# Kernel tuning notes

Measured on AMD Instinct MI355X. Metric: run time of the kernel, lower is better.

## Reference

```python
import jax, jax.numpy as jnp
import numpy as np

N = 50000       # nodes
E = 800000      # edges
IN, H, OUT = 256, 512, 64


def gcn_conv(x, src, dst, norm, W, b, n_nodes):
    # PyG GCNConv: linear transform first, then normalized scatter-add aggregation.
    xw = x @ W                                   # [N, H]
    msg = xw[src] * norm[:, None]                # [E+N, H] gathered, normalized messages
    out = jax.ops.segment_sum(msg, dst, num_segments=n_nodes)
    return out + b


def setup_inputs() -> dict:
    key = jax.random.key(0)
    ks = jax.random.split(key, 8)
    x = jax.random.normal(ks[0], (N, IN), dtype=jnp.float32)
    edge_index = jax.random.randint(ks[1], (2, E), 0, N, dtype=jnp.int64)
    W1 = jax.random.normal(ks[2], (IN, H), dtype=jnp.float32) * (1.0 / np.sqrt(IN))
    b1 = jnp.zeros((H,), dtype=jnp.float32)
    W2 = jax.random.normal(ks[3], (H, H), dtype=jnp.float32) * (1.0 / np.sqrt(H))
    b2 = jnp.zeros((H,), dtype=jnp.float32)
    Wl = jax.random.normal(ks[4], (H, OUT), dtype=jnp.float32) * (1.0 / np.sqrt(H))
    bl = jnp.zeros((OUT,), dtype=jnp.float32)
    return {"x": x, "edge_index": edge_index, "W1": W1, "b1": b1,
            "W2": W2, "b2": b2, "Wl": Wl, "bl": bl}


def reference(x, edge_index, W1, b1, W2, b2, Wl, bl):
    n = x.shape[0]
    loop = jnp.arange(n, dtype=edge_index.dtype)
    src = jnp.concatenate([edge_index[0], loop])     # add self-loops
    dst = jnp.concatenate([edge_index[1], loop])
    # symmetric normalization D^-1/2 (A+I) D^-1/2
    deg = jax.ops.segment_sum(jnp.ones_like(dst, dtype=x.dtype), dst, num_segments=n)
    dinv = jnp.where(deg > 0, jax.lax.rsqrt(jnp.maximum(deg, 1.0)), 0.0)
    norm = dinv[src] * dinv[dst]                      # [E+N]

    h = jax.nn.relu(gcn_conv(x, src, dst, norm, W1, b1, n))
    # dropout omitted (deterministic eval reference)
    h = jax.nn.relu(gcn_conv(h, src, dst, norm, W2, b2, n))
    return h @ Wl + bl
```

## Files before the change

kernel.cpp:

```cpp
#include <hip/hip_runtime.h>
#include <cstdint>
#include <cstddef>

typedef unsigned short u16;
typedef __attribute__((ext_vector_type(8))) _Float16 f16x8;
typedef __attribute__((ext_vector_type(4))) float f32x4;
typedef __attribute__((ext_vector_type(2))) unsigned u32x2;
typedef __attribute__((ext_vector_type(4))) unsigned u32x4;

__device__ __forceinline__ u16 f2h(float f) {
    union { _Float16 h; u16 u; } v; v.h = (_Float16)f;
    return v.u;
}
__device__ __forceinline__ float h2f(u16 b) {
    union { u16 u; _Float16 h; } v; v.u = b;
    return (float)v.h;
}
__device__ __forceinline__ float h2f_lo(unsigned w) { return h2f((u16)(w & 0xFFFFu)); }
__device__ __forceinline__ float h2f_hi(unsigned w) { return h2f((u16)(w >> 16)); }

__device__ __forceinline__ void gload16(const u16* g, u16* l) {
    __builtin_amdgcn_global_load_lds(
        (const __attribute__((address_space(1))) void*)g,
        (__attribute__((address_space(3))) void*)l, 16, 0, 0);
}

__global__ void init_deg_kernel(float* __restrict__ deg, int n) {
    int i = blockIdx.x * blockDim.x + threadIdx.x;
    if (i < n) deg[i] = 1.0f;
}

__global__ void count_deg_kernel(const int* __restrict__ dst, float* __restrict__ deg, int e) {
    int i = blockIdx.x * blockDim.x + threadIdx.x;
    if (i < e) atomicAdd(&deg[dst[i]], 1.0f);
}

__global__ __launch_bounds__(1024)
void scan1_kernel(const float* __restrict__ deg, int* __restrict__ part, int n) {
    __shared__ int sm[1024];
    const int t = threadIdx.x;
    const int i = blockIdx.x * 1024 + t;
    sm[t] = (i < n) ? (int)deg[i] - 1 : 0;
    __syncthreads();
    for (int off = 512; off > 0; off >>= 1) {
        if (t < off) sm[t] += sm[t + off];
        __syncthreads();
    }
    if (t == 0) part[blockIdx.x] = sm[0];
}

__global__ __launch_bounds__(1024)
void scan2_kernel(int* __restrict__ part, int nb) {
    __shared__ int sm[1024];
    const int t = threadIdx.x;
    const int v = (t < nb) ? part[t] : 0;
    sm[t] = v;
    __syncthreads();
    for (int off = 1; off < 1024; off <<= 1) {
        int tv = (t >= off) ? sm[t - off] : 0;
        __syncthreads();
        sm[t] += tv;
        __syncthreads();
    }
    if (t < nb) part[t] = sm[t] - v;
}

__global__ __launch_bounds__(1024)
void scan3_kernel(const float* __restrict__ deg, const int* __restrict__ part,
                  float* __restrict__ dinv, int* __restrict__ row_start,
                  int* __restrict__ cursor, int n) {
    __shared__ int sm[1024];
    const int t = threadIdx.x;
    const int b = blockIdx.x;
    const int i = b * 1024 + t;
    int v = 0;
    float d = 1.f;
    if (i < n) {
        d = deg[i];
        v = (int)d - 1;
    }
    sm[t] = v;
    __syncthreads();
    for (int off = 1; off < 1024; off <<= 1) {
        int tv = (t >= off) ? sm[t - off] : 0;
        __syncthreads();
        sm[t] += tv;
        __syncthreads();
    }
    if (i < n) {
        row_start[i] = part[b] + sm[t] - v;
        dinv[i] = rsqrtf(d);
        cursor[i] = 0;
    }
    if (i == n - 1) row_start[n] = part[b] + sm[t];
}

__global__ void bucket_kernel(const int* __restrict__ src, const int* __restrict__ dst,
                              const int* __restrict__ row_start, int* __restrict__ cursor,
                              int* __restrict__ csr, float* __restrict__ csr_w,
                              const float* __restrict__ dinv, int e) {
    int i = blockIdx.x * blockDim.x + threadIdx.x;
    if (i < e) {
        int d = dst[i];
        int s = src[i];
        int pos = atomicAdd(&cursor[d], 1);
        int at = row_start[d] + pos;
        csr[at] = s;
        csr_w[at] = dinv[s] * dinv[d];
    }
}

__global__ void wtrans_kernel(const float* __restrict__ W, u16* __restrict__ bt, int K, int N) {
    const int k8 = K >> 3;
    const int idx = blockIdx.x * blockDim.x + threadIdx.x;
    if (idx >= N * k8) return;
    const int n = idx / k8;
    const int k0 = (idx - n * k8) * 8;
    alignas(16) u16 h8[8];
#pragma unroll
    for (int j = 0; j < 8; j++) h8[j] = f2h(W[(size_t)(k0 + j) * N + n]);
    *(uint4*)(bt + (size_t)n * K + k0) = *(const uint4*)h8;
}

__global__ void xsplit_kernel(const float* __restrict__ x, u16* __restrict__ xh, size_t total8) {
    const size_t idx = (size_t)blockIdx.x * blockDim.x + threadIdx.x;
    if (idx >= total8) return;
    const float4 v0 = *(const float4*)(x + idx * 8);
    const float4 v1 = *(const float4*)(x + idx * 8 + 4);
    alignas(16) u16 h8[8];
    h8[0] = f2h(v0.x); h8[1] = f2h(v0.y); h8[2] = f2h(v0.z); h8[3] = f2h(v0.w);
    h8[4] = f2h(v1.x); h8[5] = f2h(v1.y); h8[6] = f2h(v1.z); h8[7] = f2h(v1.w);
    *(uint4*)(xh + idx * 8) = *(const uint4*)h8;
}

__global__ __launch_bounds__(256)
void agg_x_kernel(const float* __restrict__ x, const u16* __restrict__ xh,
                  u16* __restrict__ oh,
                  const int* __restrict__ csr, const float* __restrict__ csr_w,
                  const int* __restrict__ rs, const float* __restrict__ dinv, int n) {
    const int node = blockIdx.x * 4 + (threadIdx.x >> 6);
    if (node >= n) return;
    const int lane = threadIdx.x & 63;
    const int c0 = lane * 4;
    const int beg = rs[node], end = rs[node + 1];
    float a0 = 0.f, a1 = 0.f, a2 = 0.f, a3 = 0.f;
    int i = beg;
    for (; i + 4 <= end; i += 4) {
        int s[4];
        float w[4];
        uint2 hv[4];
#pragma unroll
        for (int u = 0; u < 4; u++) {
            s[u] = __builtin_nontemporal_load(csr + i + u);
            w[u] = __builtin_nontemporal_load(csr_w + i + u);
        }
#pragma unroll
        for (int u = 0; u < 4; u++) hv[u] = *(const uint2*)(xh + (size_t)s[u] * 256 + c0);
#pragma unroll
        for (int u = 0; u < 4; u++) {
            a0 = fmaf(h2f_lo(hv[u].x), w[u], a0);
            a1 = fmaf(h2f_hi(hv[u].x), w[u], a1);
            a2 = fmaf(h2f_lo(hv[u].y), w[u], a2);
            a3 = fmaf(h2f_hi(hv[u].y), w[u], a3);
        }
    }
    for (; i < end; i++) {
        const int sv = csr[i];
        const float w = csr_w[i];
        uint2 hv = *(const uint2*)(xh + (size_t)sv * 256 + c0);
        a0 = fmaf(h2f_lo(hv.x), w, a0);
        a1 = fmaf(h2f_hi(hv.x), w, a1);
        a2 = fmaf(h2f_lo(hv.y), w, a2);
        a3 = fmaf(h2f_hi(hv.y), w, a3);
    }
    {
        const float dn = dinv[node];
        const float ws = dn * dn;
        const float4 xv = *(const float4*)(x + (size_t)node * 256 + c0);
        a0 = fmaf(xv.x, ws, a0);
        a1 = fmaf(xv.y, ws, a1);
        a2 = fmaf(xv.z, ws, a2);
        a3 = fmaf(xv.w, ws, a3);
    }
    u32x2 ho;
    ho.x = (unsigned)f2h(a0) | ((unsigned)f2h(a1) << 16);
    ho.y = (unsigned)f2h(a2) | ((unsigned)f2h(a3) << 16);
    __builtin_nontemporal_store(ho, (u32x2*)(oh + (size_t)node * 256 + c0));
}

__global__ __launch_bounds__(256)
void agg_h_kernel(const u16* __restrict__ hin, u16* __restrict__ oh,
                  const int* __restrict__ csr, const float* __restrict__ csr_w,
                  const int* __restrict__ rs, const float* __restrict__ dinv, int n) {
    const int node = blockIdx.x * 4 + (threadIdx.x >> 6);
    if (node >= n) return;
    const int lane = threadIdx.x & 63;
    const int c0 = lane * 8;
    const int beg = rs[node], end = rs[node + 1];
    float a[8];
#pragma unroll
    for (int j = 0; j < 8; j++) a[j] = 0.f;
    int i = beg;
    for (; i + 4 <= end; i += 4) {
        int s[4];
        float w[4];
        uint4 hv[4];
#pragma unroll
        for (int u = 0; u < 4; u++) {
            s[u] = __builtin_nontemporal_load(csr + i + u);
            w[u] = __builtin_nontemporal_load(csr_w + i + u);
        }
#pragma unroll
        for (int u = 0; u < 4; u++) hv[u] = *(const uint4*)(hin + (size_t)s[u] * 512 + c0);
#pragma unroll
        for (int u = 0; u < 4; u++) {
            a[0] = fmaf(h2f_lo(hv[u].x), w[u], a[0]);
            a[1] = fmaf(h2f_hi(hv[u].x), w[u], a[1]);
            a[2] = fmaf(h2f_lo(hv[u].y), w[u], a[2]);
            a[3] = fmaf(h2f_hi(hv[u].y), w[u], a[3]);
            a[4] = fmaf(h2f_lo(hv[u].z), w[u], a[4]);
            a[5] = fmaf(h2f_hi(hv[u].z), w[u], a[5]);
            a[6] = fmaf(h2f_lo(hv[u].w), w[u], a[6]);
            a[7] = fmaf(h2f_hi(hv[u].w), w[u], a[7]);
        }
    }
    for (; i < end; i++) {
        const int sv = csr[i];
        const float w = csr_w[i];
        uint4 hv = *(const uint4*)(hin + (size_t)sv * 512 + c0);
        a[0] = fmaf(h2f_lo(hv.x), w, a[0]);
        a[1] = fmaf(h2f_hi(hv.x), w, a[1]);
        a[2] = fmaf(h2f_lo(hv.y), w, a[2]);
        a[3] = fmaf(h2f_hi(hv.y), w, a[3]);
        a[4] = fmaf(h2f_lo(hv.z), w, a[4]);
        a[5] = fmaf(h2f_hi(hv.z), w, a[5]);
        a[6] = fmaf(h2f_lo(hv.w), w, a[6]);
        a[7] = fmaf(h2f_hi(hv.w), w, a[7]);
    }
    {
        const float dn = dinv[node];
        const float ws = dn * dn;
        uint4 hv = *(const uint4*)(hin + (size_t)node * 512 + c0);
        a[0] = fmaf(h2f_lo(hv.x), ws, a[0]);
        a[1] = fmaf(h2f_hi(hv.x), ws, a[1]);
        a[2] = fmaf(h2f_lo(hv.y), ws, a[2]);
        a[3] = fmaf(h2f_hi(hv.y), ws, a[3]);
        a[4] = fmaf(h2f_lo(hv.z), ws, a[4]);
        a[5] = fmaf(h2f_hi(hv.z), ws, a[5]);
        a[6] = fmaf(h2f_lo(hv.w), ws, a[6]);
        a[7] = fmaf(h2f_hi(hv.w), ws, a[7]);
    }
    u32x4 ho;
#pragma unroll
    for (int j = 0; j < 4; j++)
        ho[j] = (unsigned)f2h(a[2 * j]) | ((unsigned)f2h(a[2 * j + 1]) << 16);
    __builtin_nontemporal_store(ho, (u32x4*)(oh + (size_t)node * 512 + c0));
}

template <bool RELU, int OUTMODE>
__global__ __launch_bounds__(512)
void gemm256_kernel(const u16* __restrict__ A, const u16* __restrict__ Bt,
                    const float* __restrict__ bias,
                    float* __restrict__ Cf, u16* __restrict__ Ch,
                    int M, int K, int Nn) {
    __shared__ u16 sA[128 * 32], sB[256 * 32];

    const int gx = gridDim.x;
    const int nwg = gx * gridDim.y;
    const int orig = blockIdx.y * gx + blockIdx.x;
    const int q8 = nwg >> 3, r8 = nwg & 7;
    const int xcd = orig & 7, lin = orig >> 3;
    const int wg = (xcd < r8 ? xcd * (q8 + 1) : r8 * (q8 + 1) + (xcd - r8) * q8) + lin;
    const int mt = wg / gx;
    const int nt = wg - mt * gx;
    const int m0 = mt * 128, n0 = nt * 256;

    const int tid = threadIdx.x;
    const int lane = tid & 63;
    const int wid = tid >> 6;
    const int wm = (wid >> 2) * 64;
    const int wn = (wid & 3) * 64;

    const int srow = tid >> 2;
    const int gslot = (tid & 3) ^ ((tid >> 3) & 3);
    const int lbase = wid * 16 * 32;

    const u16* gA  = A  + (size_t)(m0 + srow) * K + gslot * 8;
    const u16* gB0 = Bt + (size_t)(n0 + srow) * K + gslot * 8;
    const u16* gB1 = Bt + (size_t)(n0 + 128 + srow) * K + gslot * 8;

    int offA[4], offB[4];
    const int q = lane >> 4;
#pragma unroll
    for (int i = 0; i < 4; i++) {
        int r = wm + i * 16 + (lane & 15);
        offA[i] = r * 32 + ((q ^ ((r >> 1) & 3)) * 8);
    }
#pragma unroll
    for (int j = 0; j < 4; j++) {
        int r = wn + j * 16 + (lane & 15);
        offB[j] = r * 32 + ((q ^ ((r >> 1) & 3)) * 8);
    }

    f32x4 acc[4][4];
#pragma unroll
    for (int i = 0; i < 4; i++)
#pragma unroll
        for (int j = 0; j < 4; j++) acc[i][j] = (f32x4){0.f, 0.f, 0.f, 0.f};

    auto stage = [&](int k0) {
        gload16(gA + k0, sA + lbase);
        gload16(gB0 + k0, sB + lbase);
        gload16(gB1 + k0, sB + 128 * 32 + lbase);
    };

    stage(0);
    for (int k0 = 0; k0 < K; k0 += 32) {
        __syncthreads();
        f16x8 af[4], bf[4];
#pragma unroll
        for (int i = 0; i < 4; i++) af[i] = *(const f16x8*)(sA + offA[i]);
#pragma unroll
        for (int j = 0; j < 4; j++) bf[j] = *(const f16x8*)(sB + offB[j]);
#pragma unroll
        for (int i = 0; i < 4; i++)
#pragma unroll
            for (int j = 0; j < 4; j++)
                acc[i][j] = __builtin_amdgcn_mfma_f32_16x16x32_f16(af[i], bf[j], acc[i][j], 0, 0, 0);
        __syncthreads();
        if (k0 + 32 < K) stage(k0 + 32);
    }

    const int cn = lane & 15;
    const int cm = (lane >> 4) * 4;
#pragma unroll
    for (int i = 0; i < 4; i++) {
#pragma unroll
        for (int j = 0; j < 4; j++) {
            const int col = n0 + wn + j * 16 + cn;
            const float bv = bias[col];
#pragma unroll
            for (int r = 0; r < 4; r++) {
                const int row = m0 + wm + i * 16 + cm + r;
                if (row < M) {
                    float v = acc[i][j][r] + bv;
                    if (RELU) v = fmaxf(v, 0.f);
                    if constexpr (OUTMODE == 2) {
                        Ch[(size_t)row * Nn + col] = f2h(v);
                    } else {
                        Cf[(size_t)row * Nn + col] = v;
                    }
                }
            }
        }
    }
}

template <bool RELU>
__global__ __launch_bounds__(256)
void gemm64_kernel(const u16* __restrict__ A, const u16* __restrict__ Bt,
                   const float* __restrict__ bias, float* __restrict__ Cf,
                   int M, int K, int Nn) {
    __shared__ u16 sA[128 * 32], sB[64 * 32];

    const int nwg = gridDim.y;
    const int orig = blockIdx.y;
    const int q8 = nwg >> 3, r8 = nwg & 7;
    const int xcd = orig & 7, lin = orig >> 3;
    const int wg = (xcd < r8 ? xcd * (q8 + 1) : r8 * (q8 + 1) + (xcd - r8) * q8) + lin;
    const int m0 = wg * 128, n0 = 0;

    const int tid = threadIdx.x;
    const int lane = tid & 63;
    const int wid = tid >> 6;
    const int wm = (wid >> 1) * 64;
    const int wn = (wid & 1) * 32;

    const int srow = tid >> 2;
    const int gslot = (tid & 3) ^ ((tid >> 3) & 3);
    const int lbase = wid * 16 * 32;

    const u16* gA0 = A + (size_t)(m0 + srow) * K + gslot * 8;
    const u16* gA1 = A + (size_t)(m0 + 64 + srow) * K + gslot * 8;
    const u16* gB0 = Bt + (size_t)(n0 + srow) * K + gslot * 8;

    int offA[4], offB[2];
    const int q = lane >> 4;
#pragma unroll
    for (int i = 0; i < 4; i++) {
        int r = wm + i * 16 + (lane & 15);
        offA[i] = r * 32 + ((q ^ ((r >> 1) & 3)) * 8);
    }
#pragma unroll
    for (int j = 0; j < 2; j++) {
        int r = wn + j * 16 + (lane & 15);
        offB[j] = r * 32 + ((q ^ ((r >> 1) & 3)) * 8);
    }

    f32x4 acc[4][2];
#pragma unroll
    for (int i = 0; i < 4; i++)
#pragma unroll
        for (int j = 0; j < 2; j++) acc[i][j] = (f32x4){0.f, 0.f, 0.f, 0.f};

    auto stage = [&](int k0) {
        gload16(gA0 + k0, sA + lbase);
        gload16(gA1 + k0, sA + 64 * 32 + lbase);
        gload16(gB0 + k0, sB + lbase);
    };

    stage(0);
    for (int k0 = 0; k0 < K; k0 += 32) {
        __syncthreads();
        f16x8 af[4], bf[2];
#pragma unroll
        for (int i = 0; i < 4; i++) af[i] = *(const f16x8*)(sA + offA[i]);
#pragma unroll
        for (int j = 0; j < 2; j++) bf[j] = *(const f16x8*)(sB + offB[j]);
#pragma unroll
        for (int i = 0; i < 4; i++)
#pragma unroll
            for (int j = 0; j < 2; j++)
                acc[i][j] = __builtin_amdgcn_mfma_f32_16x16x32_f16(af[i], bf[j], acc[i][j], 0, 0, 0);
        __syncthreads();
        if (k0 + 32 < K) stage(k0 + 32);
    }

    const int cn = lane & 15;
    const int cm = (lane >> 4) * 4;
#pragma unroll
    for (int i = 0; i < 4; i++) {
#pragma unroll
        for (int j = 0; j < 2; j++) {
            const int col = wn + j * 16 + cn;
            const float bv = bias[col];
#pragma unroll
            for (int r = 0; r < 4; r++) {
                const int row = m0 + wm + i * 16 + cm + r;
                if (row < M) {
                    float v = acc[i][j][r] + bv;
                    if (RELU) v = fmaxf(v, 0.f);
                    Cf[(size_t)row * Nn + col] = v;
                }
            }
        }
    }
}

extern "C" void kernel_launch(void* const* d_in, const int* in_sizes, int n_in,
                              void* d_out, int out_size, void* d_ws, size_t ws_size,
                              hipStream_t stream) {
    const float* x  = (const float*)d_in[0];
    const int*   ei = (const int*)d_in[1];
    const float* W1 = (const float*)d_in[2];
    const float* b1 = (const float*)d_in[3];
    const float* W2 = (const float*)d_in[4];
    const float* b2 = (const float*)d_in[5];
    const float* Wl = (const float*)d_in[6];
    const float* bl = (const float*)d_in[7];
    float* out = (float*)d_out;

    const int N = in_sizes[0] / 256;
    const int E = in_sizes[1] / 2;
    const int Mpad = ((N + 127) / 128) * 128;
    const int nb = (N + 1023) / 1024;
    const int* src = ei;
    const int* dst = ei + E;

    size_t off = 0;
    auto alloc = [&](size_t bytes) -> void* {
        void* p = (char*)d_ws + off;
        off += (bytes + 255) & ~(size_t)255;
        return p;
    };
    float* deg       = (float*)alloc((size_t)N * 4);
    float* dinv      = (float*)alloc((size_t)N * 4);
    int*   part      = (int*)alloc((size_t)1024 * 4);
    int*   row_start = (int*)alloc((size_t)(N + 1) * 4);
    int*   cursor    = (int*)alloc((size_t)N * 4);
    int*   csr       = (int*)alloc((size_t)E * 4);
    float* csr_w     = (float*)alloc((size_t)E * 4);
    u16*   xh        = (u16*)alloc((size_t)N * 256 * 2);
    u16*   bt1 = (u16*)alloc((size_t)512 * 256 * 2);
    u16*   bt2 = (u16*)alloc((size_t)512 * 512 * 2);
    u16*   bt3 = (u16*)alloc((size_t)64 * 512 * 2);
    u16*   slabA = (u16*)alloc((size_t)Mpad * 512 * 2);
    u16*   slabH = (u16*)alloc((size_t)Mpad * 512 * 2);
    (void)ws_size;

    u16* a1h = slabA;
    u16* a2h = slabA;
    u16* h1h = slabH;
    u16* h2h = slabH;

    init_deg_kernel<<<(N + 255) / 256, 256, 0, stream>>>(deg, N);
    count_deg_kernel<<<(E + 255) / 256, 256, 0, stream>>>(dst, deg, E);
    scan1_kernel<<<nb, 1024, 0, stream>>>(deg, part, N);
    scan2_kernel<<<1, 1024, 0, stream>>>(part, nb);
    scan3_kernel<<<nb, 1024, 0, stream>>>(deg, part, dinv, row_start, cursor, N);
    bucket_kernel<<<(E + 255) / 256, 256, 0, stream>>>(src, dst, row_start, cursor, csr, csr_w, dinv, E);

    wtrans_kernel<<<(512 * 32 + 255) / 256, 256, 0, stream>>>(W1, bt1, 256, 512);
    wtrans_kernel<<<(512 * 64 + 255) / 256, 256, 0, stream>>>(W2, bt2, 512, 512);
    wtrans_kernel<<<(64 * 64 + 255) / 256, 256, 0, stream>>>(Wl, bt3, 512, 64);
    xsplit_kernel<<<((N * 32) + 255) / 256, 256, 0, stream>>>(x, xh, (size_t)N * 32);

    agg_x_kernel<<<(N + 3) / 4, 256, 0, stream>>>(x, xh, a1h, csr, csr_w, row_start, dinv, N);
    gemm256_kernel<true, 2><<<dim3(2, Mpad / 128), 512, 0, stream>>>(
        a1h, bt1, b1, nullptr, h1h, N, 256, 512);

    agg_h_kernel<<<(N + 3) / 4, 256, 0, stream>>>(h1h, a2h, csr, csr_w, row_start, dinv, N);
    gemm256_kernel<true, 2><<<dim3(2, Mpad / 128), 512, 0, stream>>>(
        a2h, bt2, b2, nullptr, h2h, N, 512, 512);

    gemm64_kernel<false><<<dim3(1, Mpad / 128), 256, 0, stream>>>(
        h2h, bt3, bl, out, N, 512, 64);
}
```

Measured before the change: 441.1 us.

## Double-buffer LDS in gemm256 and unroll edge gather loop by eight

The 256-wide GEMM now keeps two LDS buffers and issues the global-to-LDS loads for the next K tile before computing on the current one. Explicit vmcnt waits and barriers replace the old load-after-compute ordering, so memory latency is meant to overlap with MFMA work. The gather aggregation loop over CSR edges is also unrolled from 4 to 8 to keep more gathers in flight. This doubles shared memory per block, which may lower occupancy, and adds register pressure in the aggregation kernel.

```diff
diff --git a/kernel.cpp b/kernel.cpp
--- a/kernel.cpp
+++ b/kernel.cpp
@@ -145,19 +145,19 @@
     const int beg = rs[node], end = rs[node + 1];
     float a0 = 0.f, a1 = 0.f, a2 = 0.f, a3 = 0.f;
     int i = beg;
-    for (; i + 4 <= end; i += 4) {
-        int s[4];
-        float w[4];
-        uint2 hv[4];
-#pragma unroll
-        for (int u = 0; u < 4; u++) {
+    for (; i + 8 <= end; i += 8) {
+        int s[8];
+        float w[8];
+        uint2 hv[8];
+#pragma unroll
+        for (int u = 0; u < 8; u++) {
             s[u] = __builtin_nontemporal_load(csr + i + u);
             w[u] = __builtin_nontemporal_load(csr_w + i + u);
         }
 #pragma unroll
-        for (int u = 0; u < 4; u++) hv[u] = *(const uint2*)(xh + (size_t)s[u] * 256 + c0);
-#pragma unroll
-        for (int u = 0; u < 4; u++) {
+        for (int u = 0; u < 8; u++) hv[u] = *(const uint2*)(xh + (size_t)s[u] * 256 + c0);
+#pragma unroll
+        for (int u = 0; u < 8; u++) {
             a0 = fmaf(h2f_lo(hv[u].x), w[u], a0);
             a1 = fmaf(h2f_hi(hv[u].x), w[u], a1);
             a2 = fmaf(h2f_lo(hv[u].y), w[u], a2);
@@ -263,7 +263,7 @@
                     const float* __restrict__ bias,
                     float* __restrict__ Cf, u16* __restrict__ Ch,
                     int M, int K, int Nn) {
-    __shared__ u16 sA[128 * 32], sB[256 * 32];
+    __shared__ u16 sA[2][128 * 32], sB[2][256 * 32];
 
     const int gx = gridDim.x;
     const int nwg = gx * gridDim.y;
@@ -272,8 +272,8 @@
     const int xcd = orig & 7, lin = orig >> 3;
     const int wg = (xcd < r8 ? xcd * (q8 + 1) : r8 * (q8 + 1) + (xcd - r8) * q8) + lin;
     const int mt = wg / gx;
-    const int nt = wg - mt * gx;
-    const int m0 = mt * 128, n0 = nt * 256;
+    const int nt_ = wg - mt * gx;
+    const int m0 = mt * 128, n0 = nt_ * 256;
 
     const int tid = threadIdx.x;
     const int lane = tid & 63;
@@ -308,27 +308,36 @@
 #pragma unroll
         for (int j = 0; j < 4; j++) acc[i][j] = (f32x4){0.f, 0.f, 0.f, 0.f};
 
-    auto stage = [&](int k0) {
-        gload16(gA + k0, sA + lbase);
-        gload16(gB0 + k0, sB + lbase);
-        gload16(gB1 + k0, sB + 128 * 32 + lbase);
+    auto stage = [&](int k0, int b) {
+        gload16(gA + k0, sA[b] + lbase);
+        gload16(gB0 + k0, sB[b] + lbase);
+        gload16(gB1 + k0, sB[b] + 128 * 32 + lbase);
     };
 
-    stage(0);
-    for (int k0 = 0; k0 < K; k0 += 32) {
-        __syncthreads();
-        f16x8 af[4], bf[4];
-#pragma unroll
-        for (int i = 0; i < 4; i++) af[i] = *(const f16x8*)(sA + offA[i]);
-#pragma unroll
-        for (int j = 0; j < 4; j++) bf[j] = *(const f16x8*)(sB + offB[j]);
+    const int ntiles = K >> 5;
+    stage(0, 0);
+    for (int t = 0; t < ntiles; ++t) {
+        const int cur = t & 1;
+        __builtin_amdgcn_s_barrier();
+        if (t + 1 < ntiles) {
+            stage((t + 1) << 5, cur ^ 1);
+            asm volatile("s_waitcnt vmcnt(3)" ::: "memory");
+        } else {
+            asm volatile("s_waitcnt vmcnt(0)" ::: "memory");
+        }
+        __builtin_amdgcn_s_barrier();
+        __builtin_amdgcn_sched_barrier(0);
+
+        f16x8 af[4], bf4[4];
+#pragma unroll
+        for (int i = 0; i < 4; i++) af[i] = *(const f16x8*)(sA[cur] + offA[i]);
+#pragma unroll
+        for (int j = 0; j < 4; j++) bf4[j] = *(const f16x8*)(sB[cur] + offB[j]);
 #pragma unroll
         for (int i = 0; i < 4; i++)
 #pragma unroll
             for (int j = 0; j < 4; j++)
-                acc[i][j] = __builtin_amdgcn_mfma_f32_16x16x32_f16(af[i], bf[j], acc[i][j], 0, 0, 0);
-        __syncthreads();
-        if (k0 + 32 < K) stage(k0 + 32);
+                acc[i][j] = __builtin_amdgcn_mfma_f32_16x16x32_f16(af[i], bf4[j], acc[i][j], 0, 0, 0);
     }
 
     const int cn = lane & 15;
@@ -412,16 +421,16 @@
     stage(0);
     for (int k0 = 0; k0 < K; k0 += 32) {
         __syncthreads();
-        f16x8 af[4], bf[2];
+        f16x8 af[4], bf4[2];
 #pragma unroll
         for (int i = 0; i < 4; i++) af[i] = *(const f16x8*)(sA + offA[i]);
 #pragma unroll
-        for (int j = 0; j < 2; j++) bf[j] = *(const f16x8*)(sB + offB[j]);
+        for (int j = 0; j < 2; j++) bf4[j] = *(const f16x8*)(sB + offB[j]);
 #pragma unroll
         for (int i = 0; i < 4; i++)
 #pragma unroll
             for (int j = 0; j < 2; j++)
-                acc[i][j] = __builtin_amdgcn_mfma_f32_16x16x32_f16(af[i], bf[j], acc[i][j], 0, 0, 0);
+                acc[i][j] = __builtin_amdgcn_mfma_f32_16x16x32_f16(af[i], bf4[j], acc[i][j], 0, 0, 0);
         __syncthreads();
         if (k0 + 32 < K) stage(k0 + 32);
     }
```

Result: no change. 444.3 us (+0.7%).
